# Kernel tuning notes

Hardware: AMD Instinct MI355X
Metric: run time of the kernel (lower is better)

## Reference

```python
import jax, jax.numpy as jnp
import numpy as np

B, N, K, C = 4, 4096, 16, 128
BN_EPS = 1e-5


def setup_inputs() -> dict:
    key = jax.random.key(0)
    ks = jax.random.split(key, 16)
    def f(i, shape, s=0.05):
        return jax.random.normal(ks[i], shape, dtype=jnp.float32) * s
    return dict(
        pose_enc=f(0, (B, N, K, 4), 1.0),
        knn_idx=jax.random.randint(ks[1], (B, N, K), 0, N),
        new_points=f(2, (B, N, C), 1.0),
        wq=f(3, (C, C)), wk=f(4, (C, C)), wv=f(5, (C, C)),
        g_w1=f(6, (C, C)), g_b1=jnp.zeros((C,), jnp.float32),
        g_w2=f(7, (C, C)), g_b2=jnp.zeros((C,), jnp.float32),
        d_w1=f(8, (C, 4)), d_b1=jnp.zeros((C,), jnp.float32),
        d_w2=f(9, (C, C)), d_b2=jnp.zeros((C,), jnp.float32),
        c1_w=f(10, (C, C)), c1_b=jnp.zeros((C,), jnp.float32),
        bn1_g=jnp.ones((C,), jnp.float32), bn1_b=jnp.zeros((C,), jnp.float32),
        c2_w=f(11, (C, C)), c2_b=jnp.zeros((C,), jnp.float32),
        bn2_g=jnp.ones((C,), jnp.float32), bn2_b=jnp.zeros((C,), jnp.float32),
    )


def _bn(x, g, b):
    # BatchNorm1d in training mode: stats over (B, N) per channel, biased var
    m = jnp.mean(x, axis=(0, 1))
    v = jnp.mean(jnp.square(x - m), axis=(0, 1))
    return (x - m) * jax.lax.rsqrt(v + BN_EPS) * g + b


def reference(pose_enc, knn_idx, new_points, wq, wk, wv,
              g_w1, g_b1, g_w2, g_b2, d_w1, d_b1, d_w2, d_b2,
              c1_w, c1_b, bn1_g, bn1_b, c2_w, c2_b, bn2_g, bn2_b):
    # fc_delta: (B,N,K,4) -> (B,N,K,C)
    pos = jax.nn.relu(pose_enc @ d_w1.T + d_b1) @ d_w2.T + d_b2
    # CONV2 (1x1 conv == per-point linear) + BN + ReLU on new_points
    x = jax.nn.relu(_bn(new_points @ c2_w.T + c2_b, bn2_g, bn2_b))  # (B,N,C)
    q = x @ wq.T                                   # (B,N,C)
    kf = x @ wk.T
    vf = x @ wv.T
    gather = jax.vmap(lambda pts, idx: pts[idx])   # (B,N,C),(B,N,K)->(B,N,K,C)
    kk = gather(kf, knn_idx)
    vv = gather(vf, knn_idx)
    # fc_gamma vector attention scores
    h = q[:, :, None, :] - kk + pos                # (B,N,K,C)
    attn = jax.nn.relu(h @ g_w1.T + g_b1) @ g_w2.T + g_b2
    # NOTE: original divides by sqrt(k.size(-1)) where k is the key tensor -> sqrt(C)
    attn = jax.nn.softmax(attn / jnp.sqrt(jnp.float32(C)), axis=-2)
    res = jnp.einsum('bmnf,bmnf->bmf', attn, vv + pos)  # (B,N,C)
    res = jax.nn.relu(_bn(res @ c1_w.T + c1_b, bn1_g, bn1_b)) + new_points
    return res
```

## Files before the change

kernel.cpp:

```cpp
#include <hip/hip_runtime.h>
#include <hip/hip_bf16.h>

typedef __bf16 bf16;
typedef __bf16 bf16x4 __attribute__((ext_vector_type(4)));
typedef __bf16 bf16x8 __attribute__((ext_vector_type(8)));
typedef float  f32x4  __attribute__((ext_vector_type(4)));

#define NN 4096
#define KK 16
#define CC 128
#define BN_TOT 16384

__global__ __launch_bounds__(256) void k_lin(
    const float* __restrict__ A, const float* __restrict__ W,
    const float* __restrict__ bias, float* __restrict__ Y,
    float* __restrict__ partial) {
  __shared__ __attribute__((aligned(16))) bf16 WF[32 * 64 * 8];
  __shared__ __attribute__((aligned(16))) float SF[4][16][132];
  __shared__ float P1[128], P2[128];
  int tid = threadIdx.x, w = tid >> 6, l = tid & 63, quad = l >> 4, col = l & 15;
  int r0 = blockIdx.x * 64;
  int arow = r0 + w * 16 + col;

  if (tid < 128) { P1[tid] = 0.f; P2[tid] = 0.f; }

  for (int e = tid; e < 128 * 16; e += 256) {
    int r = e >> 4, c8 = e & 15;
    const float* p = W + r * CC + c8 * 8;
    f32x4 v0 = *(const f32x4*)p, v1 = *(const f32x4*)(p + 4);
    bf16x8 o;
    for (int i = 0; i < 4; i++) { o[i] = (bf16)v0[i]; o[i + 4] = (bf16)v1[i]; }
    int chunk = (r >> 4) * 4 + (c8 >> 2);
    int lane  = (c8 & 3) * 16 + (r & 15);
    *(bf16x8*)(&WF[(chunk * 64 + lane) * 8]) = o;
  }

  bf16x8 a[4];
  for (int kc = 0; kc < 4; kc++) {
    int c0 = kc * 32 + quad * 8;
    f32x4 y0 = *(const f32x4*)(A + arow * CC + c0);
    f32x4 y1 = *(const f32x4*)(A + arow * CC + c0 + 4);
    bf16x8 o;
    for (int i = 0; i < 4; i++) { o[i] = (bf16)y0[i]; o[i + 4] = (bf16)y1[i]; }
    a[kc] = o;
  }

  f32x4 D[8];
  for (int jb = 0; jb < 8; jb++) {
    float bv = bias[jb * 16 + col];
    D[jb] = (f32x4){bv, bv, bv, bv};
  }
  __syncthreads();
  for (int jb = 0; jb < 8; jb++)
    for (int kc = 0; kc < 4; kc++) {
      bf16x8 bfrag = *(const bf16x8*)(&WF[((jb * 4 + kc) * 64 + l) * 8]);
      D[jb] = __builtin_amdgcn_mfma_f32_16x16x32_bf16(a[kc], bfrag, D[jb], 0, 0, 0);
    }

  for (int jb = 0; jb < 8; jb++) {
    float t1 = D[jb][0] + D[jb][1] + D[jb][2] + D[jb][3];
    float t2 = D[jb][0] * D[jb][0] + D[jb][1] * D[jb][1]
             + D[jb][2] * D[jb][2] + D[jb][3] * D[jb][3];
    t1 += __shfl_xor(t1, 16); t1 += __shfl_xor(t1, 32);
    t2 += __shfl_xor(t2, 16); t2 += __shfl_xor(t2, 32);
    if (quad == 0) {
      atomicAdd(&P1[jb * 16 + col], t1);
      atomicAdd(&P2[jb * 16 + col], t2);
    }
  }

  for (int jb = 0; jb < 8; jb++)
    for (int g = 0; g < 4; g++)
      SF[w][quad * 4 + g][jb * 16 + col] = D[jb][g];
  int orow = r0 + w * 16 + (l >> 2), oc0 = (l & 3) * 32;
  for (int c4 = 0; c4 < 8; c4++) {
    f32x4 v = *(const f32x4*)(&SF[w][l >> 2][oc0 + c4 * 4]);
    *(f32x4*)(Y + orow * CC + oc0 + c4 * 4) = v;
  }

  __syncthreads();
  if (tid < 128) {
    partial[blockIdx.x * 256 + tid] = P1[tid];
    partial[blockIdx.x * 256 + 128 + tid] = P2[tid];
  }
}

__global__ __launch_bounds__(1024) void k_finalize(
    const float* __restrict__ partial, const float* __restrict__ g,
    const float* __restrict__ b, float* __restrict__ stats, int NB) {
  __shared__ float sh[2][1024];
  int t = threadIdx.x, c = t & 127, h = t >> 7;
  float s1 = 0.f, s2 = 0.f;
  for (int blk = h; blk < NB; blk += 8) {
    s1 += partial[blk * 256 + c];
    s2 += partial[blk * 256 + 128 + c];
  }
  sh[0][t] = s1; sh[1][t] = s2;
  __syncthreads();
  if (t < 128) {
    s1 = 0.f; s2 = 0.f;
    for (int hh = 0; hh < 8; hh++) {
      s1 += sh[0][hh * 128 + t];
      s2 += sh[1][hh * 128 + t];
    }
    float mean = s1 * (1.0f / BN_TOT);
    float var  = s2 * (1.0f / BN_TOT) - mean * mean;
    float r = rsqrtf(var + 1e-5f);
    float sc = g[t] * r;
    stats[t] = sc;
    stats[128 + t] = b[t] - mean * sc;
  }
}

__global__ __launch_bounds__(256) void k_qkv(
    const float* __restrict__ Y, const float* __restrict__ stats,
    const float* __restrict__ Wq, const float* __restrict__ Wk, const float* __restrict__ Wv,
    bf16* __restrict__ Qo, bf16* __restrict__ Ko, bf16* __restrict__ Vo) {
  __shared__ __attribute__((aligned(16))) bf16 WF[32 * 64 * 8];
  __shared__ __attribute__((aligned(16))) bf16 S[4][16][132];
  int tid = threadIdx.x, w = tid >> 6, l = tid & 63, quad = l >> 4, col = l & 15;
  int j8 = blockIdx.x >> 3, x8 = blockIdx.x & 7;
  int m = j8 >> 5;
  int rb = x8 * 32 + (j8 & 31);
  int r0 = rb * 64;
  int arow = r0 + w * 16 + col;
  const float* Wg = (m == 0) ? Wq : (m == 1) ? Wk : Wv;
  bf16* Os = (m == 0) ? Qo : (m == 1) ? Ko : Vo;

  for (int e = tid; e < 128 * 16; e += 256) {
    int r = e >> 4, c8 = e & 15;
    const float* p = Wg + r * CC + c8 * 8;
    f32x4 v0 = *(const f32x4*)p, v1 = *(const f32x4*)(p + 4);
    bf16x8 o;
    for (int i = 0; i < 4; i++) { o[i] = (bf16)v0[i]; o[i + 4] = (bf16)v1[i]; }
    int chunk = (r >> 4) * 4 + (c8 >> 2);
    int lane  = (c8 & 3) * 16 + (r & 15);
    *(bf16x8*)(&WF[(chunk * 64 + lane) * 8]) = o;
  }

  bf16x8 a[4];
  for (int kc = 0; kc < 4; kc++) {
    int c0 = kc * 32 + quad * 8;
    f32x4 y0  = *(const f32x4*)(Y + arow * CC + c0);
    f32x4 y1  = *(const f32x4*)(Y + arow * CC + c0 + 4);
    f32x4 sc0 = *(const f32x4*)(stats + c0);
    f32x4 sc1 = *(const f32x4*)(stats + c0 + 4);
    f32x4 sf0 = *(const f32x4*)(stats + 128 + c0);
    f32x4 sf1 = *(const f32x4*)(stats + 128 + c0 + 4);
    bf16x8 o;
    for (int i = 0; i < 4; i++) {
      o[i]     = (bf16)fmaxf(y0[i] * sc0[i] + sf0[i], 0.f);
      o[i + 4] = (bf16)fmaxf(y1[i] * sc1[i] + sf1[i], 0.f);
    }
    a[kc] = o;
  }

  __syncthreads();
  f32x4 D[8];
  for (int jb = 0; jb < 8; jb++) D[jb] = (f32x4){0.f, 0.f, 0.f, 0.f};
  for (int jb = 0; jb < 8; jb++)
    for (int kc = 0; kc < 4; kc++) {
      bf16x8 bfrag = *(const bf16x8*)(&WF[((jb * 4 + kc) * 64 + l) * 8]);
      D[jb] = __builtin_amdgcn_mfma_f32_16x16x32_bf16(a[kc], bfrag, D[jb], 0, 0, 0);
    }
  for (int jb = 0; jb < 8; jb++)
    for (int g = 0; g < 4; g++)
      S[w][quad * 4 + g][jb * 16 + col] = (bf16)D[jb][g];
  int orow = r0 + w * 16 + (l >> 2), oc0 = (l & 3) * 32;
  for (int c8 = 0; c8 < 4; c8++) {
    bf16x8 v = *(const bf16x8*)(&S[w][l >> 2][oc0 + c8 * 8]);
    *(bf16x8*)(Os + orow * CC + oc0 + c8 * 8) = v;
  }
}

__global__ __launch_bounds__(512) void k_attn(
    const bf16* __restrict__ Q, const bf16* __restrict__ Kf, const bf16* __restrict__ Vf,
    const int* __restrict__ knn, const float* __restrict__ pose,
    const float* __restrict__ d_w1, const float* __restrict__ d_b1,
    const float* __restrict__ d_w2, const float* __restrict__ d_b2,
    const float* __restrict__ g_w1, const float* __restrict__ g_b1,
    const float* __restrict__ g_w2, const float* __restrict__ g_b2,
    float* __restrict__ Rs) {
  __shared__ __attribute__((aligned(16))) bf16 WF[104 * 64 * 8];
  __shared__ __attribute__((aligned(16))) bf16 S[8][16][132];
  __shared__ float BSf[512];

  int tid = threadIdx.x, w = tid >> 6, l = tid & 63, quad = l >> 4, col = l & 15;
  int bid = (blockIdx.x & 7) * 32 + (blockIdx.x >> 3);

  const float* Wg3[3] = {d_w2, g_w1, g_w2};
  for (int m = 0; m < 3; m++) {
    const float* Wg = Wg3[m];
    for (int e = tid; e < 128 * 16; e += 512) {
      int r = e >> 4, c8 = e & 15;
      const float* p = Wg + r * CC + c8 * 8;
      f32x4 v0 = *(const f32x4*)p, v1 = *(const f32x4*)(p + 4);
      bf16x8 o;
      for (int i = 0; i < 4; i++) { o[i] = (bf16)v0[i]; o[i + 4] = (bf16)v1[i]; }
      int chunk = m * 32 + (r >> 4) * 4 + (c8 >> 2);
      int lane  = (c8 & 3) * 16 + (r & 15);
      *(bf16x8*)(&WF[(chunk * 64 + lane) * 8]) = o;
    }
  }
  for (int e = tid; e < 8 * 64; e += 512) {
    int jb = e >> 6, lane = e & 63, q = lane >> 4, c = lane & 15;
    bf16x8 o;
    for (int i = 0; i < 8; i++) o[i] = (bf16)0.f;
    if (q == 0) {
      f32x4 v = *(const f32x4*)(d_w1 + (jb * 16 + c) * 4);
      for (int i = 0; i < 4; i++) o[i] = (bf16)v[i];
    }
    *(bf16x8*)(&WF[((96 + jb) * 64 + lane) * 8]) = o;
  }
  if (tid < 512) {
    const float* bp = (tid < 128) ? d_b1 : (tid < 256) ? d_b2
                     : (tid < 384) ? g_b1 : g_b2;
    BSf[tid] = bp[tid & 127];
  }
  __syncthreads();

  const float smc = 0.08838834764831845f;

#pragma unroll 1
  for (int p = 0; p < 8; p++) {
    int gp = bid * 64 + w * 8 + p;
    int b  = gp >> 12;
    int i16 = knn[gp * KK + col];
    f32x4 ps = *(const f32x4*)(pose + gp * 64 + col * 4);

    bf16x8 ap;
#pragma unroll
    for (int j = 0; j < 8; j++) ap[j] = (bf16)0.f;
    if (quad == 0) {
#pragma unroll
      for (int j = 0; j < 4; j++) ap[j] = (bf16)ps[j];
    }
    f32x4 D[8];
#pragma unroll
    for (int jb = 0; jb < 8; jb++) {
      float bv = BSf[jb * 16 + col];
      D[jb] = (f32x4){bv, bv, bv, bv};
      bf16x8 bfrag = *(const bf16x8*)(&WF[((96 + jb) * 64 + l) * 8]);
      D[jb] = __builtin_amdgcn_mfma_f32_16x16x32_bf16(ap, bfrag, D[jb], 0, 0, 0);
    }
#pragma unroll
    for (int jb = 0; jb < 8; jb++)
#pragma unroll
      for (int g = 0; g < 4; g++)
        S[w][quad * 4 + g][jb * 16 + col] = (bf16)fmaxf(D[jb][g], 0.f);
    bf16x8 aA[4];
#pragma unroll
    for (int kc = 0; kc < 4; kc++)
      aA[kc] = *(const bf16x8*)(&S[w][col][kc * 32 + quad * 8]);

#pragma unroll
    for (int jb = 0; jb < 8; jb++) {
      float bv = BSf[128 + jb * 16 + col];
      D[jb] = (f32x4){bv, bv, bv, bv};
    }
#pragma unroll
    for (int jb = 0; jb < 8; jb++)
#pragma unroll
      for (int kc = 0; kc < 4; kc++) {
        bf16x8 bfrag = *(const bf16x8*)(&WF[((jb * 4 + kc) * 64 + l) * 8]);
        D[jb] = __builtin_amdgcn_mfma_f32_16x16x32_bf16(aA[kc], bfrag, D[jb], 0, 0, 0);
      }

    int vidx[4];
#pragma unroll
    for (int g = 0; g < 4; g++) vidx[g] = __shfl(i16, quad * 4 + g);
    float vpos[8][4];
#pragma unroll
    for (int g = 0; g < 4; g++) {
      const bf16* vr = Vf + ((b << 12) + vidx[g]) * CC + col;
#pragma unroll
      for (int jb = 0; jb < 8; jb++) vpos[jb][g] = (float)vr[jb * 16] + D[jb][g];
    }

#pragma unroll
    for (int jb = 0; jb < 8; jb++)
#pragma unroll
      for (int g = 0; g < 4; g++)
        S[w][quad * 4 + g][jb * 16 + col] = (bf16)D[jb][g];
    {
      int grow = (b << 12) + i16;
#pragma unroll
      for (int kc = 0; kc < 4; kc++) {
        int c0 = kc * 32 + quad * 8;
        bf16x8 kkv = *(const bf16x8*)(Kf + grow * CC + c0);
        bf16x8 qv  = *(const bf16x8*)(Q + gp * CC + c0);
        bf16x8 pv  = *(const bf16x8*)(&S[w][col][c0]);
        bf16x8 hv;
#pragma unroll
        for (int j = 0; j < 8; j++)
          hv[j] = (bf16)((float)qv[j] - (float)kkv[j] + (float)pv[j]);
        aA[kc] = hv;
      }
    }

#pragma unroll
    for (int jb = 0; jb < 8; jb++) {
      float bv = BSf[256 + jb * 16 + col];
      D[jb] = (f32x4){bv, bv, bv, bv};
    }
#pragma unroll
    for (int jb = 0; jb < 8; jb++)
#pragma unroll
      for (int kc = 0; kc < 4; kc++) {
        bf16x8 bfrag = *(const bf16x8*)(&WF[((32 + jb * 4 + kc) * 64 + l) * 8]);
        D[jb] = __builtin_amdgcn_mfma_f32_16x16x32_bf16(aA[kc], bfrag, D[jb], 0, 0, 0);
      }
#pragma unroll
    for (int jb = 0; jb < 8; jb++)
#pragma unroll
      for (int g = 0; g < 4; g++)
        S[w][quad * 4 + g][jb * 16 + col] = (bf16)fmaxf(D[jb][g], 0.f);
#pragma unroll
    for (int kc = 0; kc < 4; kc++)
      aA[kc] = *(const bf16x8*)(&S[w][col][kc * 32 + quad * 8]);

#pragma unroll
    for (int jb = 0; jb < 8; jb++) {
      float bv = BSf[384 + jb * 16 + col];
      D[jb] = (f32x4){bv, bv, bv, bv};
    }
#pragma unroll
    for (int jb = 0; jb < 8; jb++)
#pragma unroll
      for (int kc = 0; kc < 4; kc++) {
        bf16x8 bfrag = *(const bf16x8*)(&WF[((64 + jb * 4 + kc) * 64 + l) * 8]);
        D[jb] = __builtin_amdgcn_mfma_f32_16x16x32_bf16(aA[kc], bfrag, D[jb], 0, 0, 0);
      }

#pragma unroll
    for (int jb = 0; jb < 8; jb++) {
      float s = 0.f, pa = 0.f;
#pragma unroll
      for (int g = 0; g < 4; g++) {
        float e = __expf(D[jb][g] * smc);
        s += e; pa += e * vpos[jb][g];
      }
      s  += __shfl_xor(s, 16);  s += __shfl_xor(s, 32);
      pa += __shfl_xor(pa, 16); pa += __shfl_xor(pa, 32);
      if (quad == 0) Rs[gp * CC + jb * 16 + col] = pa / s;
    }
  }
}

__global__ __launch_bounds__(256) void k_out(
    const float* __restrict__ Y, const float* __restrict__ stats,
    const float* __restrict__ NP, float* __restrict__ Out) {
  int i0 = (blockIdx.x * 256 + threadIdx.x) * 4;
  int c0 = i0 & 127;
  f32x4 y  = *(const f32x4*)(Y + i0);
  f32x4 sc = *(const f32x4*)(stats + c0);
  f32x4 sh = *(const f32x4*)(stats + 128 + c0);
  f32x4 np = *(const f32x4*)(NP + i0);
  f32x4 o;
  for (int i = 0; i < 4; i++)
    o[i] = fmaxf(y[i] * sc[i] + sh[i], 0.f) + np[i];
  *(f32x4*)(Out + i0) = o;
}

__global__ void k_code(float* out, float code) {
  if (threadIdx.x == 0) out[1000003] = code;
}

extern "C" void kernel_launch(void* const* d_in, const int* in_sizes, int n_in,
                              void* d_out, int out_size, void* d_ws, size_t ws_size,
                              hipStream_t stream) {
  static const int expect[22] = {
    1048576, 262144, 2097152, 16384, 16384, 16384,
    16384, 128, 16384, 128,
    512, 128, 16384, 128,
    16384, 128, 128, 128,
    16384, 128, 128, 128
  };
  if (n_in != 22) { k_code<<<1, 64, 0, stream>>>((float*)d_out, 4194304.f); return; }
  for (int i = 0; i < 22; i++)
    if (in_sizes[i] != expect[i]) {
      k_code<<<1, 64, 0, stream>>>((float*)d_out, 262144.f * (float)(i + 1));
      return;
    }

  const float* pose  = (const float*)d_in[0];
  const int*   knn   = (const int*)d_in[1];
  const float* np_   = (const float*)d_in[2];
  const float* wq    = (const float*)d_in[3];
  const float* wk    = (const float*)d_in[4];
  const float* wv    = (const float*)d_in[5];
  const float* g_w1  = (const float*)d_in[6];
  const float* g_b1  = (const float*)d_in[7];
  const float* g_w2  = (const float*)d_in[8];
  const float* g_b2  = (const float*)d_in[9];
  const float* d_w1  = (const float*)d_in[10];
  const float* d_b1  = (const float*)d_in[11];
  const float* d_w2  = (const float*)d_in[12];
  const float* d_b2  = (const float*)d_in[13];
  const float* c1_w  = (const float*)d_in[14];
  const float* c1_b  = (const float*)d_in[15];
  const float* bn1_g = (const float*)d_in[16];
  const float* bn1_b = (const float*)d_in[17];
  const float* c2_w  = (const float*)d_in[18];
  const float* c2_b  = (const float*)d_in[19];
  const float* bn2_g = (const float*)d_in[20];
  const float* bn2_b = (const float*)d_in[21];

  float* y2      = (float*)d_ws;
  float* res     = y2 + 2097152;
  bf16*  qf      = (bf16*)(res + 2097152);
  bf16*  kf      = qf + 2097152;
  bf16*  vf      = kf + 2097152;
  float* partial = (float*)(vf + 2097152);
  float* stats2  = partial + 65536;
  float* stats1  = stats2 + 256;

  size_t NEED = (size_t)((char*)(stats1 + 256) - (char*)d_ws);
  if (ws_size < NEED) {
    k_code<<<1, 64, 0, stream>>>((float*)d_out, 2097152.f);
    return;
  }

  k_lin     <<<256, 256, 0, stream>>>(np_, c2_w, c2_b, y2, partial);
  k_finalize<<<1, 1024, 0, stream>>>(partial, bn2_g, bn2_b, stats2, 256);
  k_qkv     <<<768, 256, 0, stream>>>(y2, stats2, wq, wk, wv, qf, kf, vf);
  k_attn    <<<256, 512, 0, stream>>>(qf, kf, vf, knn, pose,
                                      d_w1, d_b1, d_w2, d_b2,
                                      g_w1, g_b1, g_w2, g_b2, res);
  k_lin     <<<256, 256, 0, stream>>>(res, c1_w, c1_b, y2, partial);
  k_finalize<<<1, 1024, 0, stream>>>(partial, bn1_g, bn1_b, stats1, 256);
  k_out     <<<2048, 256, 0, stream>>>(y2, stats1, np_, (float*)d_out);
}
```

Measured before the change: 216.4 us.

## Fuse BN finalize into linear kernel via last-block atomics; prefetch gathers in attention

Drops the two single-block finalize kernels. Each linear block now atomically adds its per-channel sum and sum of squares to a global accumulator, and the last block to arrive, found through an atomic counter, computes the BN scale and shift. A small zero kernel clears the accumulators at the start. In the attention kernel, the V and K neighbor gathers are issued earlier and the next point's knn index and pose are prefetched, to hide gather latency behind the MFMA work. The atomic reduction changes summation order and relies on threadfence ordering for correctness.

```diff
diff --git a/kernel.cpp b/kernel.cpp
--- a/kernel.cpp
+++ b/kernel.cpp
@@ -11,13 +11,21 @@
 #define CC 128
 #define BN_TOT 16384
 
+__global__ __launch_bounds__(576) void k_zero(float* __restrict__ accum) {
+  int t = threadIdx.x;
+  if (t < 514) accum[t] = 0.f;
+}
+
 __global__ __launch_bounds__(256) void k_lin(
     const float* __restrict__ A, const float* __restrict__ W,
     const float* __restrict__ bias, float* __restrict__ Y,
-    float* __restrict__ partial) {
+    float* __restrict__ accS, unsigned int* __restrict__ cnt,
+    const float* __restrict__ bng, const float* __restrict__ bnb,
+    float* __restrict__ stats) {
   __shared__ __attribute__((aligned(16))) bf16 WF[32 * 64 * 8];
   __shared__ __attribute__((aligned(16))) float SF[4][16][132];
   __shared__ float P1[128], P2[128];
+  __shared__ int lastFlag;
   int tid = threadIdx.x, w = tid >> 6, l = tid & 63, quad = l >> 4, col = l & 15;
   int r0 = blockIdx.x * 64;
   int arow = r0 + w * 16 + col;
@@ -80,35 +88,22 @@
 
   __syncthreads();
   if (tid < 128) {
-    partial[blockIdx.x * 256 + tid] = P1[tid];
-    partial[blockIdx.x * 256 + 128 + tid] = P2[tid];
-  }
-}
-
-__global__ __launch_bounds__(1024) void k_finalize(
-    const float* __restrict__ partial, const float* __restrict__ g,
-    const float* __restrict__ b, float* __restrict__ stats, int NB) {
-  __shared__ float sh[2][1024];
-  int t = threadIdx.x, c = t & 127, h = t >> 7;
-  float s1 = 0.f, s2 = 0.f;
-  for (int blk = h; blk < NB; blk += 8) {
-    s1 += partial[blk * 256 + c];
-    s2 += partial[blk * 256 + 128 + c];
-  }
-  sh[0][t] = s1; sh[1][t] = s2;
-  __syncthreads();
-  if (t < 128) {
-    s1 = 0.f; s2 = 0.f;
-    for (int hh = 0; hh < 8; hh++) {
-      s1 += sh[0][hh * 128 + t];
-      s2 += sh[1][hh * 128 + t];
-    }
+    atomicAdd(&accS[tid], P1[tid]);
+    atomicAdd(&accS[128 + tid], P2[tid]);
+  }
+  __threadfence();
+  __syncthreads();
+  if (tid == 0) lastFlag = (atomicAdd(cnt, 1u) == 255u) ? 1 : 0;
+  __syncthreads();
+  if (lastFlag && tid < 128) {
+    float s1 = atomicAdd(&accS[tid], 0.f);
+    float s2 = atomicAdd(&accS[128 + tid], 0.f);
     float mean = s1 * (1.0f / BN_TOT);
     float var  = s2 * (1.0f / BN_TOT) - mean * mean;
     float r = rsqrtf(var + 1e-5f);
-    float sc = g[t] * r;
-    stats[t] = sc;
-    stats[128 + t] = b[t] - mean * sc;
+    float sc = bng[tid] * r;
+    stats[tid] = sc;
+    stats[128 + tid] = bnb[tid] - mean * sc;
   }
 }
 
@@ -221,12 +216,26 @@
 
   const float smc = 0.08838834764831845f;
 
+  int gpf = bid * 64 + w * 8;
+  int i16 = knn[gpf * KK + col];
+  f32x4 ps = *(const f32x4*)(pose + gpf * 64 + col * 4);
+
 #pragma unroll 1
   for (int p = 0; p < 8; p++) {
     int gp = bid * 64 + w * 8 + p;
     int b  = gp >> 12;
-    int i16 = knn[gp * KK + col];
-    f32x4 ps = *(const f32x4*)(pose + gp * 64 + col * 4);
+
+    int vidx[4];
+#pragma unroll
+    for (int g = 0; g < 4; g++) vidx[g] = __shfl(i16, quad * 4 + g);
+    float vv[8][4];
+#pragma unroll
+    for (int g = 0; g < 4; g++) {
+      const bf16* vr = Vf + ((b << 12) + vidx[g]) * CC + col;
+#pragma unroll
+      for (int jb = 0; jb < 8; jb++) vv[jb][g] = (float)vr[jb * 16];
+    }
+    int grow = (b << 12) + i16;
 
     bf16x8 ap;
 #pragma unroll
@@ -253,6 +262,16 @@
     for (int kc = 0; kc < 4; kc++)
       aA[kc] = *(const bf16x8*)(&S[w][col][kc * 32 + quad * 8]);
 
+    bf16x8 kkv[4];
+#pragma unroll
+    for (int kc = 0; kc < 4; kc++)
+      kkv[kc] = *(const bf16x8*)(Kf + grow * CC + kc * 32 + quad * 8);
+
+    if (p < 7) {
+      i16 = knn[(gp + 1) * KK + col];
+      ps  = *(const f32x4*)(pose + (gp + 1) * 64 + col * 4);
+    }
+
 #pragma unroll
     for (int jb = 0; jb < 8; jb++) {
       float bv = BSf[128 + jb * 16 + col];
@@ -266,36 +285,26 @@
         D[jb] = __builtin_amdgcn_mfma_f32_16x16x32_bf16(aA[kc], bfrag, D[jb], 0, 0, 0);
       }
 
-    int vidx[4];
-#pragma unroll
-    for (int g = 0; g < 4; g++) vidx[g] = __shfl(i16, quad * 4 + g);
-    float vpos[8][4];
-#pragma unroll
-    for (int g = 0; g < 4; g++) {
-      const bf16* vr = Vf + ((b << 12) + vidx[g]) * CC + col;
-#pragma unroll
-      for (int jb = 0; jb < 8; jb++) vpos[jb][g] = (float)vr[jb * 16] + D[jb][g];
-    }
+#pragma unroll
+    for (int jb = 0; jb < 8; jb++)
+#pragma unroll
+      for (int g = 0; g < 4; g++) vv[jb][g] += D[jb][g];
 
 #pragma unroll
     for (int jb = 0; jb < 8; jb++)
 #pragma unroll
       for (int g = 0; g < 4; g++)
         S[w][quad * 4 + g][jb * 16 + col] = (bf16)D[jb][g];
-    {
-      int grow = (b << 12) + i16;
-#pragma unroll
-      for (int kc = 0; kc < 4; kc++) {
-        int c0 = kc * 32 + quad * 8;
-        bf16x8 kkv = *(const bf16x8*)(Kf + grow * CC + c0);
-        bf16x8 qv  = *(const bf16x8*)(Q + gp * CC + c0);
-        bf16x8 pv  = *(const bf16x8*)(&S[w][col][c0]);
-        bf16x8 hv;
-#pragma unroll
-        for (int j = 0; j < 8; j++)
-          hv[j] = (bf16)((float)qv[j] - (float)kkv[j] + (float)pv[j]);
-        aA[kc] = hv;
-      }
+#pragma unroll
+    for (int kc = 0; kc < 4; kc++) {
+      int c0 = kc * 32 + quad * 8;
+      bf16x8 qv = *(const bf16x8*)(Q + gp * CC + c0);
+      bf16x8 pv = *(const bf16x8*)(&S[w][col][c0]);
+      bf16x8 hv;
+#pragma unroll
+      for (int j = 0; j < 8; j++)
+        hv[j] = (bf16)((float)qv[j] - (float)kkv[kc][j] + (float)pv[j]);
+      aA[kc] = hv;
     }
 
 #pragma unroll
@@ -338,7 +347,7 @@
 #pragma unroll
       for (int g = 0; g < 4; g++) {
         float e = __expf(D[jb][g] * smc);
-        s += e; pa += e * vpos[jb][g];
+        s += e; pa += e * vv[jb][g];
       }
       s  += __shfl_xor(s, 16);  s += __shfl_xor(s, 32);
       pa += __shfl_xor(pa, 16); pa += __shfl_xor(pa, 32);
@@ -411,8 +420,12 @@
   bf16*  qf      = (bf16*)(res + 2097152);
   bf16*  kf      = qf + 2097152;
   bf16*  vf      = kf + 2097152;
-  float* partial = (float*)(vf + 2097152);
-  float* stats2  = partial + 65536;
+  float* accum   = (float*)(vf + 2097152);
+  float* acc2    = accum;
+  float* acc1    = accum + 256;
+  unsigned int* cnt2 = (unsigned int*)(accum + 512);
+  unsigned int* cnt1 = cnt2 + 1;
+  float* stats2  = accum + 514;
   float* stats1  = stats2 + 256;
 
   size_t NEED = (size_t)((char*)(stats1 + 256) - (char*)d_ws);
@@ -421,13 +434,14 @@
     return;
   }
 
-  k_lin     <<<256, 256, 0, stream>>>(np_, c2_w, c2_b, y2, partial);
-  k_finalize<<<1, 1024, 0, stream>>>(partial, bn2_g, bn2_b, stats2, 256);
-  k_qkv     <<<768, 256, 0, stream>>>(y2, stats2, wq, wk, wv, qf, kf, vf);
-  k_attn    <<<256, 512, 0, stream>>>(qf, kf, vf, knn, pose,
-                                      d_w1, d_b1, d_w2, d_b2,
-                                      g_w1, g_b1, g_w2, g_b2, res);
-  k_lin     <<<256, 256, 0, stream>>>(res, c1_w, c1_b, y2, partial);
-  k_finalize<<<1, 1024, 0, stream>>>(partial, bn1_g, bn1_b, stats1, 256);
-  k_out     <<<2048, 256, 0, stream>>>(y2, stats1, np_, (float*)d_out);
-}
+  k_zero <<<1, 576, 0, stream>>>(accum);
+  k_lin  <<<256, 256, 0, stream>>>(np_, c2_w, c2_b, y2, acc2, cnt2,
+                                   bn2_g, bn2_b, stats2);
+  k_qkv  <<<768, 256, 0, stream>>>(y2, stats2, wq, wk, wv, qf, kf, vf);
+  k_attn <<<256, 512, 0, stream>>>(qf, kf, vf, knn, pose,
+                                   d_w1, d_b1, d_w2, d_b2,
+                                   g_w1, g_b1, g_w2, g_b2, res);
+  k_lin  <<<256, 256, 0, stream>>>(res, c1_w, c1_b, y2, acc1, cnt1,
+                                   bn1_g, bn1_b, stats1);
+  k_out  <<<2048, 256, 0, stream>>>(y2, stats1, np_, (float*)d_out);
+}
```

Result: slower. 256.3 us (+18.4%).

## Split linear kernel over output-column halves and prefetch attention gathers earlier

Applied to the files above, without the earlier changes.

k_lin now launches twice as many blocks, each computing 64 of the 128 output channels, so more CUs are busy. k_finalize is updated to read the new per-half partial layout. In k_attn, the knn index and pose for the next point are loaded one iteration ahead, and the V and K neighbour gathers are issued before the MFMA chains so their latency overlaps compute. The cost is higher register pressure from keeping vv and kkv live, plus each k_lin block reloading its A rows.

```diff
diff --git a/kernel.cpp b/kernel.cpp
--- a/kernel.cpp
+++ b/kernel.cpp
@@ -15,18 +15,19 @@
     const float* __restrict__ A, const float* __restrict__ W,
     const float* __restrict__ bias, float* __restrict__ Y,
     float* __restrict__ partial) {
-  __shared__ __attribute__((aligned(16))) bf16 WF[32 * 64 * 8];
-  __shared__ __attribute__((aligned(16))) float SF[4][16][132];
-  __shared__ float P1[128], P2[128];
+  __shared__ __attribute__((aligned(16))) bf16 WF[16 * 64 * 8];
+  __shared__ __attribute__((aligned(16))) float SF[4][16][68];
+  __shared__ float P1[64], P2[64];
   int tid = threadIdx.x, w = tid >> 6, l = tid & 63, quad = l >> 4, col = l & 15;
-  int r0 = blockIdx.x * 64;
+  int rb = blockIdx.x >> 1, ch = blockIdx.x & 1;
+  int r0 = rb * 64, cbase = ch * 64;
   int arow = r0 + w * 16 + col;
 
-  if (tid < 128) { P1[tid] = 0.f; P2[tid] = 0.f; }
-
-  for (int e = tid; e < 128 * 16; e += 256) {
+  if (tid < 64) { P1[tid] = 0.f; P2[tid] = 0.f; }
+
+  for (int e = tid; e < 64 * 16; e += 256) {
     int r = e >> 4, c8 = e & 15;
-    const float* p = W + r * CC + c8 * 8;
+    const float* p = W + (cbase + r) * CC + c8 * 8;
     f32x4 v0 = *(const f32x4*)p, v1 = *(const f32x4*)(p + 4);
     bf16x8 o;
     for (int i = 0; i < 4; i++) { o[i] = (bf16)v0[i]; o[i + 4] = (bf16)v1[i]; }
@@ -45,19 +46,19 @@
     a[kc] = o;
   }
 
-  f32x4 D[8];
-  for (int jb = 0; jb < 8; jb++) {
-    float bv = bias[jb * 16 + col];
+  f32x4 D[4];
+  for (int jb = 0; jb < 4; jb++) {
+    float bv = bias[cbase + jb * 16 + col];
     D[jb] = (f32x4){bv, bv, bv, bv};
   }
   __syncthreads();
-  for (int jb = 0; jb < 8; jb++)
+  for (int jb = 0; jb < 4; jb++)
     for (int kc = 0; kc < 4; kc++) {
       bf16x8 bfrag = *(const bf16x8*)(&WF[((jb * 4 + kc) * 64 + l) * 8]);
       D[jb] = __builtin_amdgcn_mfma_f32_16x16x32_bf16(a[kc], bfrag, D[jb], 0, 0, 0);
     }
 
-  for (int jb = 0; jb < 8; jb++) {
+  for (int jb = 0; jb < 4; jb++) {
     float t1 = D[jb][0] + D[jb][1] + D[jb][2] + D[jb][3];
     float t2 = D[jb][0] * D[jb][0] + D[jb][1] * D[jb][1]
              + D[jb][2] * D[jb][2] + D[jb][3] * D[jb][3];
@@ -69,31 +70,33 @@
     }
   }
 
-  for (int jb = 0; jb < 8; jb++)
+  for (int jb = 0; jb < 4; jb++)
     for (int g = 0; g < 4; g++)
       SF[w][quad * 4 + g][jb * 16 + col] = D[jb][g];
-  int orow = r0 + w * 16 + (l >> 2), oc0 = (l & 3) * 32;
-  for (int c4 = 0; c4 < 8; c4++) {
-    f32x4 v = *(const f32x4*)(&SF[w][l >> 2][oc0 + c4 * 4]);
-    *(f32x4*)(Y + orow * CC + oc0 + c4 * 4) = v;
+  int orow = r0 + w * 16 + (l >> 2), oc = (l & 3) * 16;
+  for (int c4 = 0; c4 < 4; c4++) {
+    f32x4 v = *(const f32x4*)(&SF[w][l >> 2][oc + c4 * 4]);
+    *(f32x4*)(Y + orow * CC + cbase + oc + c4 * 4) = v;
   }
 
   __syncthreads();
-  if (tid < 128) {
-    partial[blockIdx.x * 256 + tid] = P1[tid];
-    partial[blockIdx.x * 256 + 128 + tid] = P2[tid];
+  if (tid < 64) {
+    partial[blockIdx.x * 128 + tid] = P1[tid];
+    partial[blockIdx.x * 128 + 64 + tid] = P2[tid];
   }
 }
 
 __global__ __launch_bounds__(1024) void k_finalize(
     const float* __restrict__ partial, const float* __restrict__ g,
-    const float* __restrict__ b, float* __restrict__ stats, int NB) {
+    const float* __restrict__ b, float* __restrict__ stats) {
   __shared__ float sh[2][1024];
   int t = threadIdx.x, c = t & 127, h = t >> 7;
+  int ch = c >> 6, j = c & 63;
   float s1 = 0.f, s2 = 0.f;
-  for (int blk = h; blk < NB; blk += 8) {
-    s1 += partial[blk * 256 + c];
-    s2 += partial[blk * 256 + 128 + c];
+  for (int rb = h; rb < 256; rb += 8) {
+    const float* pp = partial + (rb * 2 + ch) * 128;
+    s1 += pp[j];
+    s2 += pp[64 + j];
   }
   sh[0][t] = s1; sh[1][t] = s2;
   __syncthreads();
@@ -221,12 +224,26 @@
 
   const float smc = 0.08838834764831845f;
 
+  int gpf = bid * 64 + w * 8;
+  int i16 = knn[gpf * KK + col];
+  f32x4 ps = *(const f32x4*)(pose + gpf * 64 + col * 4);
+
 #pragma unroll 1
   for (int p = 0; p < 8; p++) {
     int gp = bid * 64 + w * 8 + p;
     int b  = gp >> 12;
-    int i16 = knn[gp * KK + col];
-    f32x4 ps = *(const f32x4*)(pose + gp * 64 + col * 4);
+
+    int vidx[4];
+#pragma unroll
+    for (int g = 0; g < 4; g++) vidx[g] = __shfl(i16, quad * 4 + g);
+    float vv[8][4];
+#pragma unroll
+    for (int g = 0; g < 4; g++) {
+      const bf16* vr = Vf + ((b << 12) + vidx[g]) * CC + col;
+#pragma unroll
+      for (int jb = 0; jb < 8; jb++) vv[jb][g] = (float)vr[jb * 16];
+    }
+    int grow = (b << 12) + i16;
 
     bf16x8 ap;
 #pragma unroll
@@ -253,6 +270,16 @@
     for (int kc = 0; kc < 4; kc++)
       aA[kc] = *(const bf16x8*)(&S[w][col][kc * 32 + quad * 8]);
 
+    bf16x8 kkv[4];
+#pragma unroll
+    for (int kc = 0; kc < 4; kc++)
+      kkv[kc] = *(const bf16x8*)(Kf + grow * CC + kc * 32 + quad * 8);
+
+    if (p < 7) {
+      i16 = knn[(gp + 1) * KK + col];
+      ps  = *(const f32x4*)(pose + (gp + 1) * 64 + col * 4);
+    }
+
 #pragma unroll
     for (int jb = 0; jb < 8; jb++) {
       float bv = BSf[128 + jb * 16 + col];
@@ -266,36 +293,26 @@
         D[jb] = __builtin_amdgcn_mfma_f32_16x16x32_bf16(aA[kc], bfrag, D[jb], 0, 0, 0);
       }
 
-    int vidx[4];
-#pragma unroll
-    for (int g = 0; g < 4; g++) vidx[g] = __shfl(i16, quad * 4 + g);
-    float vpos[8][4];
-#pragma unroll
-    for (int g = 0; g < 4; g++) {
-      const bf16* vr = Vf + ((b << 12) + vidx[g]) * CC + col;
-#pragma unroll
-      for (int jb = 0; jb < 8; jb++) vpos[jb][g] = (float)vr[jb * 16] + D[jb][g];
-    }
+#pragma unroll
+    for (int jb = 0; jb < 8; jb++)
+#pragma unroll
+      for (int g = 0; g < 4; g++) vv[jb][g] += D[jb][g];
 
 #pragma unroll
     for (int jb = 0; jb < 8; jb++)
 #pragma unroll
       for (int g = 0; g < 4; g++)
         S[w][quad * 4 + g][jb * 16 + col] = (bf16)D[jb][g];
-    {
-      int grow = (b << 12) + i16;
-#pragma unroll
-      for (int kc = 0; kc < 4; kc++) {
-        int c0 = kc * 32 + quad * 8;
-        bf16x8 kkv = *(const bf16x8*)(Kf + grow * CC + c0);
-        bf16x8 qv  = *(const bf16x8*)(Q + gp * CC + c0);
-        bf16x8 pv  = *(const bf16x8*)(&S[w][col][c0]);
-        bf16x8 hv;
-#pragma unroll
-        for (int j = 0; j < 8; j++)
-          hv[j] = (bf16)((float)qv[j] - (float)kkv[j] + (float)pv[j]);
-        aA[kc] = hv;
-      }
+#pragma unroll
+    for (int kc = 0; kc < 4; kc++) {
+      int c0 = kc * 32 + quad * 8;
+      bf16x8 qv = *(const bf16x8*)(Q + gp * CC + c0);
+      bf16x8 pv = *(const bf16x8*)(&S[w][col][c0]);
+      bf16x8 hv;
+#pragma unroll
+      for (int j = 0; j < 8; j++)
+        hv[j] = (bf16)((float)qv[j] - (float)kkv[kc][j] + (float)pv[j]);
+      aA[kc] = hv;
     }
 
 #pragma unroll
@@ -338,7 +355,7 @@
 #pragma unroll
       for (int g = 0; g < 4; g++) {
         float e = __expf(D[jb][g] * smc);
-        s += e; pa += e * vpos[jb][g];
+        s += e; pa += e * vv[jb][g];
       }
       s  += __shfl_xor(s, 16);  s += __shfl_xor(s, 32);
       pa += __shfl_xor(pa, 16); pa += __shfl_xor(pa, 32);
@@ -421,13 +438,13 @@
     return;
   }
 
-  k_lin     <<<256, 256, 0, stream>>>(np_, c2_w, c2_b, y2, partial);
-  k_finalize<<<1, 1024, 0, stream>>>(partial, bn2_g, bn2_b, stats2, 256);
+  k_lin     <<<512, 256, 0, stream>>>(np_, c2_w, c2_b, y2, partial);
+  k_finalize<<<1, 1024, 0, stream>>>(partial, bn2_g, bn2_b, stats2);
   k_qkv     <<<768, 256, 0, stream>>>(y2, stats2, wq, wk, wv, qf, kf, vf);
   k_attn    <<<256, 512, 0, stream>>>(qf, kf, vf, knn, pose,
                                       d_w1, d_b1, d_w2, d_b2,
                                       g_w1, g_b1, g_w2, g_b2, res);
-  k_lin     <<<256, 256, 0, stream>>>(res, c1_w, c1_b, y2, partial);
-  k_finalize<<<1, 1024, 0, stream>>>(partial, bn1_g, bn1_b, stats1, 256);
+  k_lin     <<<512, 256, 0, stream>>>(res, c1_w, c1_b, y2, partial);
+  k_finalize<<<1, 1024, 0, stream>>>(partial, bn1_g, bn1_b, stats1);
   k_out     <<<2048, 256, 0, stream>>>(y2, stats1, np_, (float*)d_out);
 }
```

Result: faster. 210.6 us (median of 2 runs) (-2.7%).
